# Kernel tuning notes

Measured on AMD Instinct MI355X. Metric: run time of the kernel, lower is better.

The kernel has to match this reference:

```python
import jax, jax.numpy as jnp
import numpy as np

B, S, H = 2, 2048, 2048
NH, NKV, HD = 16, 4, 128
GROUPS = NH // NKV  # 4
ROPE_BASE = 10000.0


def _rope_tables(seq_len, dim):
    inv_freq = 1.0 / (ROPE_BASE ** (jnp.arange(0, dim, 2, dtype=jnp.float32) / dim))
    t = jnp.arange(seq_len, dtype=jnp.float32)
    freqs = jnp.outer(t, inv_freq)            # [S, HD/2]
    emb = jnp.concatenate([freqs, freqs], -1)  # [S, HD]
    return jnp.cos(emb), jnp.sin(emb)


def _rotate_half(x):
    x1, x2 = x[..., : x.shape[-1] // 2], x[..., x.shape[-1] // 2:]
    return jnp.concatenate([-x2, x1], axis=-1)


def setup_inputs() -> dict:
    key = jax.random.key(0)
    ks = jax.random.split(key, 5)
    hidden_states = jax.random.normal(ks[0], (B, S, H), dtype=jnp.float32)
    wq = jax.random.normal(ks[1], (H, NH * HD), dtype=jnp.float32) * 0.02
    wk = jax.random.normal(ks[2], (H, NKV * HD), dtype=jnp.float32) * 0.02
    wv = jax.random.normal(ks[3], (H, NKV * HD), dtype=jnp.float32) * 0.02
    wo = jax.random.normal(ks[4], (NH * HD, H), dtype=jnp.float32) * 0.02
    # additive causal mask [1,1,S,S]
    causal = jnp.tril(jnp.ones((S, S), dtype=bool))
    attention_mask = jnp.where(causal, 0.0, jnp.finfo(jnp.float32).min)[None, None]
    return {"hidden_states": hidden_states, "attention_mask": attention_mask,
            "wq": wq, "wk": wk, "wv": wv, "wo": wo}


def reference(hidden_states, attention_mask, wq, wk, wv, wo):
    b, s, _ = hidden_states.shape
    # projections -> [B, heads, S, HD]
    q = (hidden_states @ wq).reshape(b, s, NH, HD).transpose(0, 2, 1, 3)
    k = (hidden_states @ wk).reshape(b, s, NKV, HD).transpose(0, 2, 1, 3)
    v = (hidden_states @ wv).reshape(b, s, NKV, HD).transpose(0, 2, 1, 3)
    cos, sin = _rope_tables(s, HD)             # [S, HD]
    cos = cos[None, None]; sin = sin[None, None]
    q = q * cos + _rotate_half(q) * sin
    k = k * cos + _rotate_half(k) * sin
    # GQA: repeat kv heads (matches repeat_interleave on dim=1)
    k = jnp.repeat(k, GROUPS, axis=1)
    v = jnp.repeat(v, GROUPS, axis=1)
    scores = jnp.einsum("bhqd,bhkd->bhqk", q, k) / jnp.sqrt(jnp.float32(HD))
    scores = scores + attention_mask
    probs = jax.nn.softmax(scores.astype(jnp.float32), axis=-1).astype(q.dtype)
    attn = jnp.einsum("bhqk,bhkd->bhqd", probs, v)
    attn = attn.transpose(0, 2, 1, 3).reshape(b, s, NH * HD)
    return attn @ wo
```

## Files before the change

kernel.cpp:

```cpp
#include <hip/hip_runtime.h>

typedef unsigned short u16;
typedef unsigned int u32;
typedef __attribute__((ext_vector_type(8))) __bf16 bf16x8;
typedef __attribute__((ext_vector_type(8))) u16 u16x8;
typedef __attribute__((ext_vector_type(4))) float f32x4;

#define B_ 2
#define S_ 2048
#define H_ 2048
#define NH_ 16
#define NKV_ 4
#define HD_ 128
#define L2E 1.4426950408889634f

__device__ __forceinline__ u16 f2bf(float f) {
  return __builtin_bit_cast(u16, static_cast<__bf16>(f));
}
__device__ __forceinline__ float bf2f(u16 v) {
  return __builtin_bit_cast(float, (u32)v << 16);
}
__device__ __forceinline__ void gl2lds16(const void* g, void* l) {
  __builtin_amdgcn_global_load_lds((const __attribute__((address_space(1))) u32*)g,
                                   (__attribute__((address_space(3))) u32*)l, 16, 0, 0);
}
__device__ __forceinline__ f32x4 mfma16(bf16x8 a, bf16x8 b, f32x4 c) {
  return __builtin_amdgcn_mfma_f32_16x16x32_bf16(a, b, c, 0, 0, 0);
}

__global__ __launch_bounds__(256) void cvt_f32_bf16(const float* __restrict__ in,
                                                    u16* __restrict__ out) {
  size_t i = ((size_t)blockIdx.x * 256 + threadIdx.x) * 8;
  const float4* p = (const float4*)(in + i);
  float4 a = p[0], b = p[1];
  u16x8 o;
  o[0] = f2bf(a.x); o[1] = f2bf(a.y); o[2] = f2bf(a.z); o[3] = f2bf(a.w);
  o[4] = f2bf(b.x); o[5] = f2bf(b.y); o[6] = f2bf(b.z); o[7] = f2bf(b.w);
  *(u16x8*)(out + i) = o;
}

__global__ __launch_bounds__(256) void transpose_f32_bf16(const float* __restrict__ in,
                                                          u16* __restrict__ out,
                                                          int R, int C) {
  __shared__ float tl[32][33];
  int bx = blockIdx.x, by = blockIdx.y;
  int tx = threadIdx.x & 31, ty = threadIdx.x >> 5;
#pragma unroll
  for (int i = 0; i < 32; i += 8)
    tl[ty + i][tx] = in[(size_t)(by * 32 + ty + i) * C + bx * 32 + tx];
  __syncthreads();
#pragma unroll
  for (int i = 0; i < 32; i += 8)
    out[(size_t)(bx * 32 + ty + i) * R + by * 32 + tx] = f2bf(tl[tx][ty + i]);
}

__global__ __launch_bounds__(256) void transpose_v(const u16* __restrict__ kvb,
                                                   u16* __restrict__ vt) {
  __shared__ u16 tl[32][33];
  int sx = blockIdx.x, dx = blockIdx.y, b = blockIdx.z;
  int tx = threadIdx.x & 31, ty = threadIdx.x >> 5;
#pragma unroll
  for (int i = 0; i < 32; i += 8)
    tl[ty + i][tx] = kvb[(size_t)(b * S_ + sx * 32 + ty + i) * 1024 + 512 + dx * 32 + tx];
  __syncthreads();
#pragma unroll
  for (int i = 0; i < 32; i += 8)
    vt[(size_t)(b * 512 + dx * 32 + ty + i) * 2048 + sx * 32 + tx] = tl[tx][ty + i];
}

__global__ __launch_bounds__(256) void rope_kernel(u16* __restrict__ buf, int rstride,
                                                   int nhshift, float scale) {
  int idx = blockIdx.x * 256 + threadIdx.x;
  int grp = idx & 7;
  int h = (idx >> 3) & ((1 << nhshift) - 1);
  int tok = idx >> (3 + nhshift);
  int s = tok & (S_ - 1);
  u16* p = buf + (size_t)tok * rstride + (h << 7) + grp * 8;
  u16x8 lo = *(u16x8*)p;
  u16x8 hi = *(u16x8*)(p + 64);
  u16x8 olo, ohi;
#pragma unroll
  for (int j = 0; j < 8; j++) {
    int i = grp * 8 + j;
    float inv = exp2f((float)i * -0.20762050593045702f);
    float ang = (float)s * inv;
    float c = cosf(ang) * scale, sn = sinf(ang) * scale;
    float xl = bf2f(lo[j]), xh = bf2f(hi[j]);
    olo[j] = f2bf(xl * c - xh * sn);
    ohi[j] = f2bf(xh * c + xl * sn);
  }
  *(u16x8*)p = olo;
  *(u16x8*)(p + 64) = ohi;
}

template <int MODE>
__global__ __launch_bounds__(256) void gemm_bt(const u16* __restrict__ A,
                                               const u16* __restrict__ BT,
                                               void* __restrict__ C0,
                                               void* __restrict__ C1,
                                               int M, int N, int K) {
  __shared__ u16 As[2 * 128 * 32];
  __shared__ u16 Bs[2 * 128 * 32];
  const int Mt = M >> 7;
  const int nwg = gridDim.x;
  int wg = (blockIdx.x & 7) * (nwg >> 3) + (blockIdx.x >> 3);
  int tm = wg % Mt, tn = wg / Mt;
  const size_t m0 = (size_t)tm << 7, n0 = (size_t)tn << 7;
  const int tid = threadIdx.x;
  const int w = tid >> 6, lane = tid & 63;
  const int g = lane >> 4, l15 = lane & 15;
  const int wr = w >> 1, wc = w & 1;

  const int r0 = tid >> 2, s0 = tid & 3;
  const int r1 = (tid + 256) >> 2, s1 = (tid + 256) & 3;
  const u16* Ar0 = A + (m0 + r0) * K + s0 * 8;
  const u16* Ar1 = A + (m0 + r1) * K + s1 * 8;
  const u16* Br0 = BT + (n0 + r0) * K + s0 * 8;
  const u16* Br1 = BT + (n0 + r1) * K + s1 * 8;

  const f32x4 Z4 = {0.f, 0.f, 0.f, 0.f};
  f32x4 acc[4][4];
#pragma unroll
  for (int m = 0; m < 4; m++)
#pragma unroll
    for (int n = 0; n < 4; n++) acc[m][n] = Z4;

  gl2lds16(Ar0, &As[w * 512]);
  gl2lds16(Ar1, &As[w * 512 + 2048]);
  gl2lds16(Br0, &Bs[w * 512]);
  gl2lds16(Br1, &Bs[w * 512 + 2048]);
  __syncthreads();

  const int nk = K >> 5;
  int cur = 0;
  for (int t = 0; t < nk; ++t) {
    if (t + 1 < nk) {
      const int k0 = (t + 1) << 5;
      const int nb = (cur ^ 1) << 12;
      gl2lds16(Ar0 + k0, &As[nb + w * 512]);
      gl2lds16(Ar1 + k0, &As[nb + w * 512 + 2048]);
      gl2lds16(Br0 + k0, &Bs[nb + w * 512]);
      gl2lds16(Br1 + k0, &Bs[nb + w * 512 + 2048]);
    }
    const int cb = cur << 12;
    bf16x8 af[4], bfr[4];
#pragma unroll
    for (int m = 0; m < 4; m++)
      af[m] = *(const bf16x8*)&As[cb + (wr * 64 + m * 16 + l15) * 32 + g * 8];
#pragma unroll
    for (int n = 0; n < 4; n++)
      bfr[n] = *(const bf16x8*)&Bs[cb + (wc * 64 + n * 16 + l15) * 32 + g * 8];
#pragma unroll
    for (int m = 0; m < 4; m++)
#pragma unroll
      for (int n = 0; n < 4; n++) acc[m][n] = mfma16(af[m], bfr[n], acc[m][n]);
    __syncthreads();
    cur ^= 1;
  }

  if (MODE == 2) {
    float* C = (float*)C0;
#pragma unroll
    for (int m = 0; m < 4; m++)
#pragma unroll
      for (int n = 0; n < 4; n++)
#pragma unroll
        for (int r = 0; r < 4; r++) {
          size_t row = m0 + wr * 64 + m * 16 + g * 4 + r;
          size_t col = n0 + wc * 64 + n * 16 + l15;
          C[row * (size_t)N + col] = acc[m][n][r];
        }
  } else {
    u16* C;
    size_t cs, cbase;
    if (n0 < 2048) { C = (u16*)C0; cs = 2048; cbase = n0; }
    else           { C = (u16*)C1; cs = 1024; cbase = n0 - 2048; }
#pragma unroll
    for (int m = 0; m < 4; m++)
#pragma unroll
      for (int n = 0; n < 4; n++)
#pragma unroll
        for (int r = 0; r < 4; r++) {
          size_t row = m0 + wr * 64 + m * 16 + g * 4 + r;
          C[row * cs + cbase + wc * 64 + n * 16 + l15] = f2bf(acc[m][n][r]);
        }
  }
}

__global__ __launch_bounds__(256) void attn_kernel(const u16* __restrict__ Qb,
                                                   const u16* __restrict__ KVb,
                                                   const u16* __restrict__ Vt,
                                                   u16* __restrict__ Ob) {
  __shared__ u16 Ks[2][64 * 128];
  __shared__ u16 Vs[2][128 * 64];
  __shared__ u16 Ps[4][16 * 72];
  const int pair = blockIdx.x, h = blockIdx.y, b = blockIdx.z;
  const int kvh = h >> 2;
  const int tid = threadIdx.x, w = tid >> 6, lane = tid & 63;
  const int g = lane >> 4, l15 = lane & 15;
  const f32x4 Z4 = {0.f, 0.f, 0.f, 0.f};
  u16x8 oneu;
#pragma unroll
  for (int j = 0; j < 8; j++) oneu[j] = 0x3f80;
  const bf16x8 ones = __builtin_bit_cast(bf16x8, oneu);

  const u16* Kbase = KVb + (size_t)b * S_ * 1024 + kvh * 128;
  const u16* Vbase = Vt + (size_t)(b * NKV_ + kvh) * HD_ * 2048;

  for (int half = 0; half < 2; ++half) {
    const int qt = half ? pair : 31 - pair;
    const int qrow0 = qt * 64 + w * 16;

    bf16x8 qf[4];
    const u16* qp = Qb + (size_t)(b * S_ + qrow0 + l15) * 2048 + h * 128;
#pragma unroll
    for (int ds = 0; ds < 4; ds++) qf[ds] = *(const bf16x8*)(qp + ds * 32 + g * 8);

    float m_r[4], l_r[4];
    f32x4 oa[8];
#pragma unroll
    for (int r = 0; r < 4; r++) { m_r[r] = -1e30f; l_r[r] = 0.f; }
#pragma unroll
    for (int n = 0; n < 8; n++) oa[n] = Z4;

    const int nt = qt + 1;
#pragma unroll
    for (int ro = 0; ro < 4; ++ro) {
      int c = ro * 256 + tid;
      int kv = c >> 4, p = c & 15;
      gl2lds16(Kbase + (size_t)kv * 1024 + 8 * (p ^ (kv & 15)), &Ks[0][ro * 2048 + w * 512]);
      int d = c >> 3, p2 = c & 7;
      gl2lds16(Vbase + (size_t)d * 2048 + 8 * (p2 ^ (d & 7)), &Vs[0][ro * 2048 + w * 512]);
    }
    __syncthreads();
    int cur = 0;

    for (int t = 0; t < nt; ++t) {
      const int kv0 = t * 64;
      if (t + 1 < nt) {
        const int nkv0 = kv0 + 64;
#pragma unroll
        for (int ro = 0; ro < 4; ++ro) {
          int c = ro * 256 + tid;
          int kv = c >> 4, p = c & 15;
          gl2lds16(Kbase + (size_t)(nkv0 + kv) * 1024 + 8 * (p ^ (kv & 15)),
                   &Ks[cur ^ 1][ro * 2048 + w * 512]);
          int d = c >> 3, p2 = c & 7;
          gl2lds16(Vbase + (size_t)d * 2048 + nkv0 + 8 * (p2 ^ (d & 7)),
                   &Vs[cur ^ 1][ro * 2048 + w * 512]);
        }
      }

      f32x4 sa[4];
#pragma unroll
      for (int c16 = 0; c16 < 4; c16++) sa[c16] = Z4;
      __builtin_amdgcn_s_setprio(1);
#pragma unroll
      for (int ds = 0; ds < 4; ++ds) {
#pragma unroll
        for (int c16 = 0; c16 < 4; ++c16) {
          bf16x8 kf = *(const bf16x8*)&Ks[cur][(c16 * 16 + l15) * 128 + ((ds * 4 + g) ^ l15) * 8];
          sa[c16] = mfma16(qf[ds], kf, sa[c16]);
        }
      }
      __builtin_amdgcn_s_setprio(0);

      if (kv0 + 63 > qrow0) {
#pragma unroll
        for (int c16 = 0; c16 < 4; c16++)
#pragma unroll
          for (int r = 0; r < 4; r++) {
            if (kv0 + c16 * 16 + l15 > qrow0 + g * 4 + r) sa[c16][r] = -1e30f;
          }
      }

      float lmax[4];
#pragma unroll
      for (int r = 0; r < 4; r++)
        lmax[r] = fmaxf(fmaxf(sa[0][r], sa[1][r]), fmaxf(sa[2][r], sa[3][r]));
      bool need = (lmax[0] > m_r[0] + 8.f) || (lmax[1] > m_r[1] + 8.f) ||
                  (lmax[2] > m_r[2] + 8.f) || (lmax[3] > m_r[3] + 8.f);
      if (__any(need)) {
        float pm[4];
#pragma unroll
        for (int r = 0; r < 4; r++) pm[r] = lmax[r];
#pragma unroll
        for (int off = 1; off < 16; off <<= 1)
#pragma unroll
          for (int r = 0; r < 4; r++) pm[r] = fmaxf(pm[r], __shfl_xor(pm[r], off));
#pragma unroll
        for (int r = 0; r < 4; r++) {
          float mn = fmaxf(m_r[r], pm[r]);
          float corr = exp2f((m_r[r] - mn) * L2E);
          m_r[r] = mn;
          l_r[r] *= corr;
#pragma unroll
          for (int n = 0; n < 8; n++) oa[n][r] *= corr;
        }
      }

#pragma unroll
      for (int c16 = 0; c16 < 4; c16++)
#pragma unroll
        for (int r = 0; r < 4; r++)
          Ps[w][(g * 4 + r) * 72 + c16 * 16 + l15] =
              f2bf(exp2f((sa[c16][r] - m_r[r]) * L2E));
      asm volatile("s_waitcnt lgkmcnt(0)" ::: "memory");
      __builtin_amdgcn_sched_barrier(0);

      f32x4 srow = Z4;
      __builtin_amdgcn_s_setprio(1);
#pragma unroll
      for (int ks = 0; ks < 2; ++ks) {
        bf16x8 pa = *(const bf16x8*)&Ps[w][l15 * 72 + ks * 32 + g * 8];
        srow = mfma16(pa, ones, srow);
#pragma unroll
        for (int n = 0; n < 8; n++) {
          bf16x8 vf = *(const bf16x8*)&Vs[cur][(n * 16 + l15) * 64 + (((ks * 4 + g) ^ (l15 & 7))) * 8];
          oa[n] = mfma16(pa, vf, oa[n]);
        }
      }
      __builtin_amdgcn_s_setprio(0);
#pragma unroll
      for (int r = 0; r < 4; r++) l_r[r] += srow[r];

      __syncthreads();
      cur ^= 1;
    }

    float inv[4];
#pragma unroll
    for (int r = 0; r < 4; r++) inv[r] = 1.0f / l_r[r];
#pragma unroll
    for (int n = 0; n < 8; n++)
#pragma unroll
      for (int r = 0; r < 4; r++) {
        size_t row = (size_t)b * S_ + qrow0 + g * 4 + r;
        Ob[row * 2048 + h * 128 + n * 16 + l15] = f2bf(oa[n][r] * inv[r]);
      }
  }
}

extern "C" void kernel_launch(void* const* d_in, const int* in_sizes, int n_in,
                              void* d_out, int out_size, void* d_ws, size_t ws_size,
                              hipStream_t stream) {
  const float* hid = (const float*)d_in[0];
  const float* wq = (const float*)d_in[2];
  const float* wk = (const float*)d_in[3];
  const float* wv = (const float*)d_in[4];
  const float* wo = (const float*)d_in[5];
  float* out = (float*)d_out;
  char* ws = (char*)d_ws;

  u16* hb     = (u16*)(ws);
  u16* wqkvT  = (u16*)(ws + (16u << 20));
  u16* Vt     = (u16*)(ws + (16u << 20));
  u16* woT    = (u16*)(ws + (20u << 20));
  u16* Qb     = (u16*)(ws + (28u << 20));
  u16* KVb    = (u16*)(ws + (44u << 20));

  cvt_f32_bf16<<<4096, 256, 0, stream>>>(hid, hb);
  transpose_f32_bf16<<<dim3(64, 64), 256, 0, stream>>>(wq, wqkvT, 2048, 2048);
  transpose_f32_bf16<<<dim3(16, 64), 256, 0, stream>>>(wk, wqkvT + (size_t)2048 * 2048, 2048, 512);
  transpose_f32_bf16<<<dim3(16, 64), 256, 0, stream>>>(wv, wqkvT + (size_t)2560 * 2048, 2048, 512);

  gemm_bt<1><<<768, 256, 0, stream>>>(hb, wqkvT, Qb, KVb, 4096, 3072, 2048);

  rope_kernel<<<2048, 256, 0, stream>>>(Qb, 2048, 4, 0.08838834764831845f);
  rope_kernel<<<512, 256, 0, stream>>>(KVb, 1024, 2, 1.0f);

  transpose_v<<<dim3(64, 16, 2), 256, 0, stream>>>(KVb, Vt);
  transpose_f32_bf16<<<dim3(64, 64), 256, 0, stream>>>(wo, woT, 2048, 2048);

  attn_kernel<<<dim3(16, 16, 2), 256, 0, stream>>>(Qb, KVb, Vt, hb);

  gemm_bt<2><<<512, 256, 0, stream>>>(hb, woT, out, nullptr, 4096, 2048, 2048);
}
```

Measured before the change: 237.9 us.

## Drop K/V double-buffering and pair scheduling; one query tile per block

The attention kernel now launches one block per query tile (1024 blocks) instead of pairing a long and a short tile per block (512 blocks). The K/V LDS tiles are single-buffered and loaded synchronously at the start of each step, and the per-thread global offsets are precomputed once. The goal is to halve LDS use so more blocks fit per CU and to spread work across more blocks. In exchange, loads no longer overlap compute within a block, and per-block work is uneven under causal masking, so the kernel relies on other resident blocks to hide latency.

```diff
diff --git a/kernel.cpp b/kernel.cpp
--- a/kernel.cpp
+++ b/kernel.cpp
@@ -191,10 +191,11 @@
                                                    const u16* __restrict__ KVb,
                                                    const u16* __restrict__ Vt,
                                                    u16* __restrict__ Ob) {
-  __shared__ u16 Ks[2][64 * 128];
-  __shared__ u16 Vs[2][128 * 64];
+  __shared__ u16 Ks[64 * 128];
+  __shared__ u16 Vs[128 * 64];
   __shared__ u16 Ps[4][16 * 72];
-  const int pair = blockIdx.x, h = blockIdx.y, b = blockIdx.z;
+  const int qt = 31 - blockIdx.x;
+  const int h = blockIdx.y, b = blockIdx.z;
   const int kvh = h >> 2;
   const int tid = threadIdx.x, w = tid >> 6, lane = tid & 63;
   const int g = lane >> 4, l15 = lane & 15;
@@ -207,138 +208,125 @@
   const u16* Kbase = KVb + (size_t)b * S_ * 1024 + kvh * 128;
   const u16* Vbase = Vt + (size_t)(b * NKV_ + kvh) * HD_ * 2048;
 
-  for (int half = 0; half < 2; ++half) {
-    const int qt = half ? pair : 31 - pair;
-    const int qrow0 = qt * 64 + w * 16;
-
-    bf16x8 qf[4];
-    const u16* qp = Qb + (size_t)(b * S_ + qrow0 + l15) * 2048 + h * 128;
-#pragma unroll
-    for (int ds = 0; ds < 4; ds++) qf[ds] = *(const bf16x8*)(qp + ds * 32 + g * 8);
-
-    float m_r[4], l_r[4];
-    f32x4 oa[8];
-#pragma unroll
-    for (int r = 0; r < 4; r++) { m_r[r] = -1e30f; l_r[r] = 0.f; }
-#pragma unroll
-    for (int n = 0; n < 8; n++) oa[n] = Z4;
-
-    const int nt = qt + 1;
+  size_t koff[4], voff[4];
+#pragma unroll
+  for (int ro = 0; ro < 4; ++ro) {
+    int c = ro * 256 + tid;
+    int kv = c >> 4, p = c & 15;
+    koff[ro] = (size_t)kv * 1024 + 8 * (p ^ (kv & 15));
+    int d = c >> 3, p2 = c & 7;
+    voff[ro] = (size_t)d * 2048 + 8 * (p2 ^ (d & 7));
+  }
+
+  const int qrow0 = qt * 64 + w * 16;
+  bf16x8 qf[4];
+  const u16* qp = Qb + (size_t)(b * S_ + qrow0 + l15) * 2048 + h * 128;
+#pragma unroll
+  for (int ds = 0; ds < 4; ds++) qf[ds] = *(const bf16x8*)(qp + ds * 32 + g * 8);
+
+  float m_r[4], l_r[4];
+  f32x4 oa[8];
+#pragma unroll
+  for (int r = 0; r < 4; r++) { m_r[r] = -1e30f; l_r[r] = 0.f; }
+#pragma unroll
+  for (int n = 0; n < 8; n++) oa[n] = Z4;
+
+  const int nt = qt + 1;
+  for (int t = 0; t < nt; ++t) {
+    const int kv0 = t * 64;
 #pragma unroll
     for (int ro = 0; ro < 4; ++ro) {
-      int c = ro * 256 + tid;
-      int kv = c >> 4, p = c & 15;
-      gl2lds16(Kbase + (size_t)kv * 1024 + 8 * (p ^ (kv & 15)), &Ks[0][ro * 2048 + w * 512]);
-      int d = c >> 3, p2 = c & 7;
-      gl2lds16(Vbase + (size_t)d * 2048 + 8 * (p2 ^ (d & 7)), &Vs[0][ro * 2048 + w * 512]);
+      gl2lds16(Kbase + (size_t)kv0 * 1024 + koff[ro], &Ks[ro * 2048 + w * 512]);
+      gl2lds16(Vbase + kv0 + voff[ro], &Vs[ro * 2048 + w * 512]);
     }
     __syncthreads();
-    int cur = 0;
-
-    for (int t = 0; t < nt; ++t) {
-      const int kv0 = t * 64;
-      if (t + 1 < nt) {
-        const int nkv0 = kv0 + 64;
-#pragma unroll
-        for (int ro = 0; ro < 4; ++ro) {
-          int c = ro * 256 + tid;
-          int kv = c >> 4, p = c & 15;
-          gl2lds16(Kbase + (size_t)(nkv0 + kv) * 1024 + 8 * (p ^ (kv & 15)),
-                   &Ks[cur ^ 1][ro * 2048 + w * 512]);
-          int d = c >> 3, p2 = c & 7;
-          gl2lds16(Vbase + (size_t)d * 2048 + nkv0 + 8 * (p2 ^ (d & 7)),
-                   &Vs[cur ^ 1][ro * 2048 + w * 512]);
+
+    f32x4 sa[4];
+#pragma unroll
+    for (int c16 = 0; c16 < 4; c16++) sa[c16] = Z4;
+    __builtin_amdgcn_s_setprio(1);
+#pragma unroll
+    for (int ds = 0; ds < 4; ++ds) {
+#pragma unroll
+      for (int c16 = 0; c16 < 4; ++c16) {
+        bf16x8 kf = *(const bf16x8*)&Ks[(c16 * 16 + l15) * 128 + ((ds * 4 + g) ^ l15) * 8];
+        sa[c16] = mfma16(qf[ds], kf, sa[c16]);
+      }
+    }
+    __builtin_amdgcn_s_setprio(0);
+
+    if (kv0 + 63 > qrow0) {
+#pragma unroll
+      for (int c16 = 0; c16 < 4; c16++)
+#pragma unroll
+        for (int r = 0; r < 4; r++) {
+          if (kv0 + c16 * 16 + l15 > qrow0 + g * 4 + r) sa[c16][r] = -1e30f;
         }
+    }
+
+    float lmax[4];
+#pragma unroll
+    for (int r = 0; r < 4; r++)
+      lmax[r] = fmaxf(fmaxf(sa[0][r], sa[1][r]), fmaxf(sa[2][r], sa[3][r]));
+    bool need = (lmax[0] > m_r[0] + 8.f) || (lmax[1] > m_r[1] + 8.f) ||
+                (lmax[2] > m_r[2] + 8.f) || (lmax[3] > m_r[3] + 8.f);
+    if (__any(need)) {
+      float pm[4];
+#pragma unroll
+      for (int r = 0; r < 4; r++) pm[r] = lmax[r];
+#pragma unroll
+      for (int off = 1; off < 16; off <<= 1)
+#pragma unroll
+        for (int r = 0; r < 4; r++) pm[r] = fmaxf(pm[r], __shfl_xor(pm[r], off));
+#pragma unroll
+      for (int r = 0; r < 4; r++) {
+        float mn = fmaxf(m_r[r], pm[r]);
+        float corr = exp2f((m_r[r] - mn) * L2E);
+        m_r[r] = mn;
+        l_r[r] *= corr;
+#pragma unroll
+        for (int n = 0; n < 8; n++) oa[n][r] *= corr;
       }
-
-      f32x4 sa[4];
-#pragma unroll
-      for (int c16 = 0; c16 < 4; c16++) sa[c16] = Z4;
-      __builtin_amdgcn_s_setprio(1);
-#pragma unroll
-      for (int ds = 0; ds < 4; ++ds) {
-#pragma unroll
-        for (int c16 = 0; c16 < 4; ++c16) {
-          bf16x8 kf = *(const bf16x8*)&Ks[cur][(c16 * 16 + l15) * 128 + ((ds * 4 + g) ^ l15) * 8];
-          sa[c16] = mfma16(qf[ds], kf, sa[c16]);
-        }
+    }
+
+#pragma unroll
+    for (int c16 = 0; c16 < 4; c16++)
+#pragma unroll
+      for (int r = 0; r < 4; r++)
+        Ps[w][(g * 4 + r) * 72 + c16 * 16 + l15] =
+            f2bf(exp2f((sa[c16][r] - m_r[r]) * L2E));
+    asm volatile("s_waitcnt lgkmcnt(0)" ::: "memory");
+    __builtin_amdgcn_sched_barrier(0);
+
+    f32x4 srow = Z4;
+    __builtin_amdgcn_s_setprio(1);
+#pragma unroll
+    for (int ks = 0; ks < 2; ++ks) {
+      bf16x8 pa = *(const bf16x8*)&Ps[w][l15 * 72 + ks * 32 + g * 8];
+      srow = mfma16(pa, ones, srow);
+#pragma unroll
+      for (int n = 0; n < 8; n++) {
+        bf16x8 vf = *(const bf16x8*)&Vs[(n * 16 + l15) * 64 + (((ks * 4 + g) ^ (l15 & 7))) * 8];
+        oa[n] = mfma16(pa, vf, oa[n]);
       }
-      __builtin_amdgcn_s_setprio(0);
-
-      if (kv0 + 63 > qrow0) {
-#pragma unroll
-        for (int c16 = 0; c16 < 4; c16++)
-#pragma unroll
-          for (int r = 0; r < 4; r++) {
-            if (kv0 + c16 * 16 + l15 > qrow0 + g * 4 + r) sa[c16][r] = -1e30f;
-          }
-      }
-
-      float lmax[4];
-#pragma unroll
-      for (int r = 0; r < 4; r++)
-        lmax[r] = fmaxf(fmaxf(sa[0][r], sa[1][r]), fmaxf(sa[2][r], sa[3][r]));
-      bool need = (lmax[0] > m_r[0] + 8.f) || (lmax[1] > m_r[1] + 8.f) ||
-                  (lmax[2] > m_r[2] + 8.f) || (lmax[3] > m_r[3] + 8.f);
-      if (__any(need)) {
-        float pm[4];
-#pragma unroll
-        for (int r = 0; r < 4; r++) pm[r] = lmax[r];
-#pragma unroll
-        for (int off = 1; off < 16; off <<= 1)
-#pragma unroll
-          for (int r = 0; r < 4; r++) pm[r] = fmaxf(pm[r], __shfl_xor(pm[r], off));
-#pragma unroll
-        for (int r = 0; r < 4; r++) {
-          float mn = fmaxf(m_r[r], pm[r]);
-          float corr = exp2f((m_r[r] - mn) * L2E);
-          m_r[r] = mn;
-          l_r[r] *= corr;
-#pragma unroll
-          for (int n = 0; n < 8; n++) oa[n][r] *= corr;
-        }
-      }
-
-#pragma unroll
-      for (int c16 = 0; c16 < 4; c16++)
-#pragma unroll
-        for (int r = 0; r < 4; r++)
-          Ps[w][(g * 4 + r) * 72 + c16 * 16 + l15] =
-              f2bf(exp2f((sa[c16][r] - m_r[r]) * L2E));
-      asm volatile("s_waitcnt lgkmcnt(0)" ::: "memory");
-      __builtin_amdgcn_sched_barrier(0);
-
-      f32x4 srow = Z4;
-      __builtin_amdgcn_s_setprio(1);
-#pragma unroll
-      for (int ks = 0; ks < 2; ++ks) {
-        bf16x8 pa = *(const bf16x8*)&Ps[w][l15 * 72 + ks * 32 + g * 8];
-        srow = mfma16(pa, ones, srow);
-#pragma unroll
-        for (int n = 0; n < 8; n++) {
-          bf16x8 vf = *(const bf16x8*)&Vs[cur][(n * 16 + l15) * 64 + (((ks * 4 + g) ^ (l15 & 7))) * 8];
-          oa[n] = mfma16(pa, vf, oa[n]);
-        }
-      }
-      __builtin_amdgcn_s_setprio(0);
-#pragma unroll
-      for (int r = 0; r < 4; r++) l_r[r] += srow[r];
-
-      __syncthreads();
-      cur ^= 1;
-    }
-
-    float inv[4];
-#pragma unroll
-    for (int r = 0; r < 4; r++) inv[r] = 1.0f / l_r[r];
-#pragma unroll
-    for (int n = 0; n < 8; n++)
-#pragma unroll
-      for (int r = 0; r < 4; r++) {
-        size_t row = (size_t)b * S_ + qrow0 + g * 4 + r;
-        Ob[row * 2048 + h * 128 + n * 16 + l15] = f2bf(oa[n][r] * inv[r]);
-      }
-  }
+    }
+    __builtin_amdgcn_s_setprio(0);
+#pragma unroll
+    for (int r = 0; r < 4; r++) l_r[r] += srow[r];
+
+    __syncthreads();
+  }
+
+  float inv[4];
+#pragma unroll
+  for (int r = 0; r < 4; r++) inv[r] = 1.0f / l_r[r];
+#pragma unroll
+  for (int n = 0; n < 8; n++)
+#pragma unroll
+    for (int r = 0; r < 4; r++) {
+      size_t row = (size_t)b * S_ + qrow0 + g * 4 + r;
+      Ob[row * 2048 + h * 128 + n * 16 + l15] = f2bf(oa[n][r] * inv[r]);
+    }
 }
 
 extern "C" void kernel_launch(void* const* d_in, const int* in_sizes, int n_in,
@@ -372,7 +360,7 @@
   transpose_v<<<dim3(64, 16, 2), 256, 0, stream>>>(KVb, Vt);
   transpose_f32_bf16<<<dim3(64, 64), 256, 0, stream>>>(wo, woT, 2048, 2048);
 
-  attn_kernel<<<dim3(16, 16, 2), 256, 0, stream>>>(Qb, KVb, Vt, hb);
+  attn_kernel<<<dim3(32, 16, 2), 256, 0, stream>>>(Qb, KVb, Vt, hb);
 
   gemm_bt<2><<<512, 256, 0, stream>>>(hb, woT, out, nullptr, 4096, 2048, 2048);
 }
```

Result: slower. 288.1 us (+21.1%).
